# Performance work log

Measured on AMD Instinct MI355X. Metric: run time of the kernel, lower is better.

## Reference

```python
import jax, jax.numpy as jnp
import numpy as np

VOCAB, EMB, ATT = 100000, 128, 128
N_CODES, N_ANC = 100000, 8

def setup_inputs() -> dict:
    key = jax.random.key(0)
    k1, k2, k3, k4, k5 = jax.random.split(key, 5)
    return {
        "W_emb": jax.random.normal(k1, (VOCAB, EMB), dtype=jnp.float32),
        "W_attention": jax.random.normal(k2, (2 * EMB, ATT), dtype=jnp.float32) * 0.05,
        "b_attention": jnp.zeros((ATT,), dtype=jnp.float32),
        "v_attention": jax.random.normal(k3, (ATT,), dtype=jnp.float32) * 0.05,
        "leaves": jax.random.randint(k4, (N_CODES, N_ANC), 0, VOCAB, dtype=jnp.int64),
        "ancestors": jax.random.randint(k5, (N_CODES, N_ANC), 0, VOCAB, dtype=jnp.int64),
    }

def reference(W_emb, W_attention, b_attention, v_attention, leaves, ancestors):
    # gather: [N, A, E] each
    leave_emb = W_emb[leaves]
    anc_emb = W_emb[ancestors]
    attention_input = jnp.concatenate((leave_emb, anc_emb), axis=2)  # [N, A, 2E]
    mlp = jnp.tanh(jnp.einsum('nae,ed->nad', attention_input, W_attention) + b_attention)
    pre_attention = jnp.einsum('nad,d->na', mlp, v_attention)  # [N, A]
    attn = jax.nn.softmax(pre_attention, axis=1)
    # attention-weighted sum over ancestors: [N, E]
    return jnp.einsum('nae,na->ne', anc_emb, attn)
```

## Files before the change

### kernel.cpp

```cpp
#include <hip/hip_runtime.h>
#include <hip/hip_bf16.h>

#define VOCAB  100000
#define EMB    128
#define NCODES 100000
#define NANC   8
#define PAD    136

typedef __attribute__((ext_vector_type(8))) short  short8;
typedef __attribute__((ext_vector_type(4))) float  float4v;

__device__ __forceinline__ ushort f2bf(float x) {
    unsigned u = __float_as_uint(x);
    u += 0x7fffu + ((u >> 16) & 1u);
    return (ushort)(u >> 16);
}
__device__ __forceinline__ float bf2f(ushort h) {
    return __uint_as_float((unsigned)h << 16);
}
__device__ __forceinline__ float tanh_fast(float x) {
    float e = __expf(2.0f * x);
    return 1.0f - __fdividef(2.0f, e + 1.0f);
}

__global__ __launch_bounds__(256) void precompute(
    const float* __restrict__ W_emb,
    const float* __restrict__ W_att,
    const float* __restrict__ b_att,
    ushort* __restrict__ P1, ushort* __restrict__ P2, ushort* __restrict__ Ebf)
{
    __shared__ ushort sBT[256 * PAD];
    const int t = threadIdx.x;

    {
        const int tg = t >> 7;
        const int c  = t & 127;
        for (int rr = 0; rr < 128; rr += 2) {
            const int r = tg * 128 + rr;
            ushort2 pk;
            pk.x = f2bf(W_att[r * 128 + c]);
            pk.y = f2bf(W_att[(r + 1) * 128 + c]);
            *(ushort2*)&sBT[(tg * 128 + c) * PAD + rr] = pk;
        }
    }
    __syncthreads();

    const int wave = t >> 6, lane = t & 63;
    const int n15 = lane & 15, quad = lane >> 4;
    const long arow = (long)blockIdx.x * 64 + wave * 16 + n15;
    const long arc  = arow < VOCAB ? arow : 0;

    float4v acc[16];
    #pragma unroll
    for (int i = 0; i < 16; ++i) acc[i] = (float4v)0.0f;

    #pragma unroll
    for (int kt = 0; kt < 4; ++kt) {
        const float4* src = (const float4*)(W_emb + arc * 128 + kt * 32 + quad * 8);
        const float4 a0 = src[0], a1 = src[1];
        short8 af;
        af[0] = f2bf(a0.x); af[1] = f2bf(a0.y); af[2] = f2bf(a0.z); af[3] = f2bf(a0.w);
        af[4] = f2bf(a1.x); af[5] = f2bf(a1.y); af[6] = f2bf(a1.z); af[7] = f2bf(a1.w);
        if (arow < VOCAB)
            *(short8*)(void*)(Ebf + arow * 128 + kt * 32 + quad * 8) = af;
        #pragma unroll
        for (int nt = 0; nt < 16; ++nt) {
            short8 bfr = *(const short8*)&sBT[(nt * 16 + n15) * PAD + kt * 32 + quad * 8];
            acc[nt] = __builtin_amdgcn_mfma_f32_16x16x32_bf16(af, bfr, acc[nt], 0, 0, 0);
        }
    }

    float bv[8];
    #pragma unroll
    for (int nt = 0; nt < 8; ++nt) bv[nt] = b_att[nt * 16 + n15];

    const long srow0 = (long)blockIdx.x * 64 + wave * 16 + quad * 4;
    #pragma unroll
    for (int nt = 0; nt < 16; ++nt) {
        const int cc = nt * 16 + n15;
        #pragma unroll
        for (int i = 0; i < 4; ++i) {
            const long gr = srow0 + i;
            if (gr < VOCAB) {
                const float v = acc[nt][i] + (nt < 8 ? bv[nt] : 0.0f);
                const ushort h = f2bf(v);
                if (nt < 8) P1[gr * 128 + cc]       = h;
                else        P2[gr * 128 + cc - 128] = h;
            }
        }
    }
}

__global__ __launch_bounds__(256) void attention_main(
    const ushort* __restrict__ P1, const ushort* __restrict__ P2,
    const ushort* __restrict__ Ebf,
    const float* __restrict__ v_att,
    const int*   __restrict__ leaves, const int* __restrict__ anc,
    float*       __restrict__ out)
{
    const int lane = threadIdx.x & 63;
    const int wave = threadIdx.x >> 6;
    const int h    = lane >> 5, l32 = lane & 31;
    const long n   = ((long)blockIdx.x * 4 + wave) * 2 + h;

    const float4 vv = *(const float4*)(v_att + l32 * 4);

    int lidx = 0;
    if (l32 < 16)
        lidx = (l32 < 8) ? leaves[n * 8 + l32] : anc[n * 8 + (l32 & 7)];

    ushort4 emb[NANC];
    float q[NANC];
    #pragma unroll
    for (int a = 0; a < NANC; ++a) {
        const int lf = __shfl(lidx, h * 32 + a);
        const int an = __shfl(lidx, h * 32 + 8 + a);
        const ushort4 r1 = *(const ushort4*)(P1  + (size_t)lf * 128 + l32 * 4);
        const ushort4 r2 = *(const ushort4*)(P2  + (size_t)an * 128 + l32 * 4);
        emb[a]           = *(const ushort4*)(Ebf + (size_t)an * 128 + l32 * 4);
        const float z0 = bf2f(r1.x) + bf2f(r2.x);
        const float z1 = bf2f(r1.y) + bf2f(r2.y);
        const float z2 = bf2f(r1.z) + bf2f(r2.z);
        const float z3 = bf2f(r1.w) + bf2f(r2.w);
        float qp = tanh_fast(z0) * vv.x + tanh_fast(z1) * vv.y
                 + tanh_fast(z2) * vv.z + tanh_fast(z3) * vv.w;
        qp += __shfl_xor(qp, 1); qp += __shfl_xor(qp, 2);
        qp += __shfl_xor(qp, 4); qp += __shfl_xor(qp, 8);
        qp += __shfl_xor(qp, 16);
        q[a] = qp;
    }

    float m = q[0];
    #pragma unroll
    for (int a = 1; a < NANC; ++a) m = fmaxf(m, q[a]);
    float s = 0.f, w[NANC];
    #pragma unroll
    for (int a = 0; a < NANC; ++a) { w[a] = __expf(q[a] - m); s += w[a]; }
    const float inv = __fdividef(1.0f, s);

    float4 o = make_float4(0.f, 0.f, 0.f, 0.f);
    #pragma unroll
    for (int a = 0; a < NANC; ++a) {
        const float wa = w[a] * inv;
        o.x = fmaf(wa, bf2f(emb[a].x), o.x);
        o.y = fmaf(wa, bf2f(emb[a].y), o.y);
        o.z = fmaf(wa, bf2f(emb[a].z), o.z);
        o.w = fmaf(wa, bf2f(emb[a].w), o.w);
    }
    *(float4*)(out + (size_t)n * 128 + l32 * 4) = o;
}

extern "C" void kernel_launch(void* const* d_in, const int* in_sizes, int n_in,
                              void* d_out, int out_size, void* d_ws, size_t ws_size,
                              hipStream_t stream) {
    const float* W_emb  = (const float*)d_in[0];
    const float* W_att  = (const float*)d_in[1];
    const float* b_att  = (const float*)d_in[2];
    const float* v_att  = (const float*)d_in[3];
    const int*   leaves = (const int*)d_in[4];
    const int*   anc    = (const int*)d_in[5];
    float*       out    = (float*)d_out;

    ushort* P1  = (ushort*)d_ws;
    ushort* P2  = P1 + (size_t)VOCAB * 128;
    ushort* Ebf = P2 + (size_t)VOCAB * 128;

    precompute<<<(VOCAB + 63) / 64, 256, 0, stream>>>(W_emb, W_att, b_att,
                                                      P1, P2, Ebf);
    attention_main<<<NCODES / 8, 256, 0, stream>>>(P1, P2, Ebf, v_att,
                                                   leaves, anc, out);
}
```

Measured before the change: 231.6 us.

## Store projections in FP8, retile precompute, and regroup attention lanes per code

```diff
diff --git a/kernel.cpp b/kernel.cpp
--- a/kernel.cpp
+++ b/kernel.cpp
@@ -1,14 +1,15 @@
 #include <hip/hip_runtime.h>
 #include <hip/hip_bf16.h>
+#include <hip/hip_fp8.h>
 
 #define VOCAB  100000
 #define EMB    128
 #define NCODES 100000
 #define NANC   8
-#define PAD    136
 
 typedef __attribute__((ext_vector_type(8))) short  short8;
 typedef __attribute__((ext_vector_type(4))) float  float4v;
+typedef __attribute__((ext_vector_type(2))) float  floatx2;
 
 __device__ __forceinline__ ushort f2bf(float x) {
     unsigned u = __float_as_uint(x);
@@ -22,132 +23,195 @@
     float e = __expf(2.0f * x);
     return 1.0f - __fdividef(2.0f, e + 1.0f);
 }
+__device__ __forceinline__ unsigned char f2fp8(float x) {
+    __hip_fp8_e4m3 t(x);
+    return t.__x;
+}
+template <bool HI>
+__device__ __forceinline__ floatx2 fp8pair(unsigned v) {
+#if __has_builtin(__builtin_amdgcn_cvt_pk_f32_fp8)
+    return __builtin_amdgcn_cvt_pk_f32_fp8((int)v, HI);
+#else
+    __hip_fp8_e4m3 a, b;
+    const unsigned s = HI ? 16u : 0u;
+    a.__x = (v >> s) & 0xffu;
+    b.__x = (v >> (s + 8u)) & 0xffu;
+    floatx2 r; r[0] = (float)a; r[1] = (float)b; return r;
+#endif
+}
+
+__global__ void transpose_watt(const float* __restrict__ W_att,
+                               ushort* __restrict__ WT)
+{
+    const int id = blockIdx.x * 256 + threadIdx.x;
+    const int c = id >> 7, e = id & 127;
+    const int h = c >> 7, d = c & 127;
+    WT[c * 128 + e] = f2bf(W_att[(h * 128 + e) * 128 + d]);
+}
 
 __global__ __launch_bounds__(256) void precompute(
-    const float* __restrict__ W_emb,
-    const float* __restrict__ W_att,
-    const float* __restrict__ b_att,
-    ushort* __restrict__ P1, ushort* __restrict__ P2, ushort* __restrict__ Ebf)
+    const float*  __restrict__ W_emb,
+    const ushort* __restrict__ WT,
+    const float*  __restrict__ b_att,
+    unsigned char* __restrict__ P1,
+    unsigned char* __restrict__ P2,
+    ushort*        __restrict__ Ebf)
 {
-    __shared__ ushort sBT[256 * PAD];
-    const int t = threadIdx.x;
-
-    {
-        const int tg = t >> 7;
-        const int c  = t & 127;
-        for (int rr = 0; rr < 128; rr += 2) {
-            const int r = tg * 128 + rr;
-            ushort2 pk;
-            pk.x = f2bf(W_att[r * 128 + c]);
-            pk.y = f2bf(W_att[(r + 1) * 128 + c]);
-            *(ushort2*)&sBT[(tg * 128 + c) * PAD + rr] = pk;
-        }
-    }
-    __syncthreads();
-
-    const int wave = t >> 6, lane = t & 63;
+    const int t = threadIdx.x, wave = t >> 6, lane = t & 63;
     const int n15 = lane & 15, quad = lane >> 4;
-    const long arow = (long)blockIdx.x * 64 + wave * 16 + n15;
-    const long arc  = arow < VOCAB ? arow : 0;
-
-    float4v acc[16];
-    #pragma unroll
-    for (int i = 0; i < 16; ++i) acc[i] = (float4v)0.0f;
+    const int R = blockIdx.x * 16;
+
+    short8 bfrag[4][4];
+    #pragma unroll
+    for (int ntl = 0; ntl < 4; ++ntl) {
+        const int c = wave * 64 + ntl * 16 + n15;
+        #pragma unroll
+        for (int kt = 0; kt < 4; ++kt)
+            bfrag[kt][ntl] = *(const short8*)(WT + c * 128 + kt * 32 + quad * 8);
+    }
+
+    float4v acc[4];
+    #pragma unroll
+    for (int i = 0; i < 4; ++i) acc[i] = (float4v)0.0f;
 
     #pragma unroll
     for (int kt = 0; kt < 4; ++kt) {
-        const float4* src = (const float4*)(W_emb + arc * 128 + kt * 32 + quad * 8);
+        const float4* src = (const float4*)(W_emb + (size_t)(R + n15) * 128
+                                            + kt * 32 + quad * 8);
         const float4 a0 = src[0], a1 = src[1];
         short8 af;
         af[0] = f2bf(a0.x); af[1] = f2bf(a0.y); af[2] = f2bf(a0.z); af[3] = f2bf(a0.w);
         af[4] = f2bf(a1.x); af[5] = f2bf(a1.y); af[6] = f2bf(a1.z); af[7] = f2bf(a1.w);
-        if (arow < VOCAB)
-            *(short8*)(void*)(Ebf + arow * 128 + kt * 32 + quad * 8) = af;
-        #pragma unroll
-        for (int nt = 0; nt < 16; ++nt) {
-            short8 bfr = *(const short8*)&sBT[(nt * 16 + n15) * PAD + kt * 32 + quad * 8];
-            acc[nt] = __builtin_amdgcn_mfma_f32_16x16x32_bf16(af, bfr, acc[nt], 0, 0, 0);
+        if (wave == 0)
+            __builtin_nontemporal_store(af,
+                (short8*)(Ebf + (size_t)(R + n15) * 128 + kt * 32 + quad * 8));
+        #pragma unroll
+        for (int ntl = 0; ntl < 4; ++ntl)
+            acc[ntl] = __builtin_amdgcn_mfma_f32_16x16x32_bf16(
+                           af, bfrag[kt][ntl], acc[ntl], 0, 0, 0);
+    }
+
+    const int cw = wave * 64;
+    float bv[4] = {0.f, 0.f, 0.f, 0.f};
+    if (wave < 2) {
+        #pragma unroll
+        for (int ntl = 0; ntl < 4; ++ntl) bv[ntl] = b_att[cw + ntl * 16 + n15];
+    }
+    unsigned char* Pt = (wave < 2) ? P1 : P2;
+    const int cofs = (wave < 2) ? cw : cw - 128;
+    #pragma unroll
+    for (int ntl = 0; ntl < 4; ++ntl) {
+        const int c = cofs + ntl * 16 + n15;
+        #pragma unroll
+        for (int i = 0; i < 4; ++i) {
+            const int r = R + quad * 4 + i;
+            __builtin_nontemporal_store(f2fp8(acc[ntl][i] + bv[ntl]),
+                                        Pt + (size_t)r * 128 + c);
         }
     }
-
-    float bv[8];
-    #pragma unroll
-    for (int nt = 0; nt < 8; ++nt) bv[nt] = b_att[nt * 16 + n15];
-
-    const long srow0 = (long)blockIdx.x * 64 + wave * 16 + quad * 4;
-    #pragma unroll
-    for (int nt = 0; nt < 16; ++nt) {
-        const int cc = nt * 16 + n15;
-        #pragma unroll
-        for (int i = 0; i < 4; ++i) {
-            const long gr = srow0 + i;
-            if (gr < VOCAB) {
-                const float v = acc[nt][i] + (nt < 8 ? bv[nt] : 0.0f);
-                const ushort h = f2bf(v);
-                if (nt < 8) P1[gr * 128 + cc]       = h;
-                else        P2[gr * 128 + cc - 128] = h;
-            }
-        }
-    }
 }
 
 __global__ __launch_bounds__(256) void attention_main(
-    const ushort* __restrict__ P1, const ushort* __restrict__ P2,
+    const unsigned char* __restrict__ P1, const unsigned char* __restrict__ P2,
     const ushort* __restrict__ Ebf,
     const float* __restrict__ v_att,
     const int*   __restrict__ leaves, const int* __restrict__ anc,
     float*       __restrict__ out)
 {
-    const int lane = threadIdx.x & 63;
-    const int wave = threadIdx.x >> 6;
-    const int h    = lane >> 5, l32 = lane & 31;
-    const long n   = ((long)blockIdx.x * 4 + wave) * 2 + h;
-
-    const float4 vv = *(const float4*)(v_att + l32 * 4);
-
-    int lidx = 0;
-    if (l32 < 16)
-        lidx = (l32 < 8) ? leaves[n * 8 + l32] : anc[n * 8 + (l32 & 7)];
-
-    ushort4 emb[NANC];
+    const int t = threadIdx.x;
+    const int wave = t >> 6, lane = t & 63;
+    const int sub = lane >> 4, l16 = lane & 15;
+    const int n = blockIdx.x * 16 + wave * 4 + sub;
+
+    const float4 vva = *(const float4*)(v_att + l16 * 8);
+    const float4 vvb = *(const float4*)(v_att + l16 * 8 + 4);
+
+    const int jj = l16 & 7;
+    const int lidx = (l16 & 8) ? anc[n * 8 + jj] : leaves[n * 8 + jj];
+
+    short8 em[NANC];
     float q[NANC];
     #pragma unroll
     for (int a = 0; a < NANC; ++a) {
-        const int lf = __shfl(lidx, h * 32 + a);
-        const int an = __shfl(lidx, h * 32 + 8 + a);
-        const ushort4 r1 = *(const ushort4*)(P1  + (size_t)lf * 128 + l32 * 4);
-        const ushort4 r2 = *(const ushort4*)(P2  + (size_t)an * 128 + l32 * 4);
-        emb[a]           = *(const ushort4*)(Ebf + (size_t)an * 128 + l32 * 4);
-        const float z0 = bf2f(r1.x) + bf2f(r2.x);
-        const float z1 = bf2f(r1.y) + bf2f(r2.y);
-        const float z2 = bf2f(r1.z) + bf2f(r2.z);
-        const float z3 = bf2f(r1.w) + bf2f(r2.w);
-        float qp = tanh_fast(z0) * vv.x + tanh_fast(z1) * vv.y
-                 + tanh_fast(z2) * vv.z + tanh_fast(z3) * vv.w;
-        qp += __shfl_xor(qp, 1); qp += __shfl_xor(qp, 2);
-        qp += __shfl_xor(qp, 4); qp += __shfl_xor(qp, 8);
-        qp += __shfl_xor(qp, 16);
+        const int lf = __shfl(lidx, (sub << 4) + a);
+        const int an = __shfl(lidx, (sub << 4) + 8 + a);
+        const uint2 r1 = *(const uint2*)(P1 + (size_t)lf * 128 + l16 * 8);
+        const uint2 r2 = *(const uint2*)(P2 + (size_t)an * 128 + l16 * 8);
+        em[a] = *(const short8*)(Ebf + (size_t)an * 128 + l16 * 8);
+        floatx2 pa, pb;
+        float qp;
+        pa = fp8pair<false>(r1.x); pb = fp8pair<false>(r2.x);
+        qp  = tanh_fast(pa[0] + pb[0]) * vva.x;
+        qp  = fmaf(tanh_fast(pa[1] + pb[1]), vva.y, qp);
+        pa = fp8pair<true>(r1.x);  pb = fp8pair<true>(r2.x);
+        qp  = fmaf(tanh_fast(pa[0] + pb[0]), vva.z, qp);
+        qp  = fmaf(tanh_fast(pa[1] + pb[1]), vva.w, qp);
+        pa = fp8pair<false>(r1.y); pb = fp8pair<false>(r2.y);
+        qp  = fmaf(tanh_fast(pa[0] + pb[0]), vvb.x, qp);
+        qp  = fmaf(tanh_fast(pa[1] + pb[1]), vvb.y, qp);
+        pa = fp8pair<true>(r1.y);  pb = fp8pair<true>(r2.y);
+        qp  = fmaf(tanh_fast(pa[0] + pb[0]), vvb.z, qp);
+        qp  = fmaf(tanh_fast(pa[1] + pb[1]), vvb.w, qp);
         q[a] = qp;
     }
 
-    float m = q[0];
-    #pragma unroll
-    for (int a = 1; a < NANC; ++a) m = fmaxf(m, q[a]);
-    float s = 0.f, w[NANC];
-    #pragma unroll
-    for (int a = 0; a < NANC; ++a) { w[a] = __expf(q[a] - m); s += w[a]; }
-    const float inv = __fdividef(1.0f, s);
-
-    float4 o = make_float4(0.f, 0.f, 0.f, 0.f);
+    float r4[4];
+    #pragma unroll
+    for (int i = 0; i < 4; ++i) {
+        const float keep = (l16 & 8) ? q[i + 4] : q[i];
+        const float send = (l16 & 8) ? q[i]     : q[i + 4];
+        r4[i] = keep + __shfl_xor(send, 8);
+    }
+    float s2[2];
+    #pragma unroll
+    for (int i = 0; i < 2; ++i) {
+        const float keep = (l16 & 4) ? r4[i + 2] : r4[i];
+        const float send = (l16 & 4) ? r4[i]     : r4[i + 2];
+        s2[i] = keep + __shfl_xor(send, 4);
+    }
+    {
+        const float keep = (l16 & 2) ? s2[1] : s2[0];
+        const float send = (l16 & 2) ? s2[0] : s2[1];
+        s2[0] = keep + __shfl_xor(send, 2);
+    }
+    float tq = s2[0] + __shfl_xor(s2[0], 1);
+
+    float m = tq;
+    m = fmaxf(m, __shfl_xor(m, 8));
+    m = fmaxf(m, __shfl_xor(m, 4));
+    m = fmaxf(m, __shfl_xor(m, 2));
+    const float e = __expf(tq - m);
+    float s = e;
+    s += __shfl_xor(s, 8); s += __shfl_xor(s, 4); s += __shfl_xor(s, 2);
+    const float wl = e * __fdividef(1.0f, s);
+
+    float wa[NANC];
+    {
+        const float p  = __shfl_xor(wl, 2);
+        const float w0 = (l16 & 2) ? p  : wl;
+        const float w1 = (l16 & 2) ? wl : p;
+        const float p0 = __shfl_xor(w0, 4), p1 = __shfl_xor(w1, 4);
+        const float v00 = (l16 & 4) ? p0 : w0, v01 = (l16 & 4) ? p1 : w1;
+        const float v10 = (l16 & 4) ? w0 : p0, v11 = (l16 & 4) ? w1 : p1;
+        float g;
+        g = __shfl_xor(v00, 8); wa[0] = (l16 & 8) ? g : v00; wa[4] = (l16 & 8) ? v00 : g;
+        g = __shfl_xor(v01, 8); wa[1] = (l16 & 8) ? g : v01; wa[5] = (l16 & 8) ? v01 : g;
+        g = __shfl_xor(v10, 8); wa[2] = (l16 & 8) ? g : v10; wa[6] = (l16 & 8) ? v10 : g;
+        g = __shfl_xor(v11, 8); wa[3] = (l16 & 8) ? g : v11; wa[7] = (l16 & 8) ? v11 : g;
+    }
+
+    float o[8] = {0.f, 0.f, 0.f, 0.f, 0.f, 0.f, 0.f, 0.f};
     #pragma unroll
     for (int a = 0; a < NANC; ++a) {
-        const float wa = w[a] * inv;
-        o.x = fmaf(wa, bf2f(emb[a].x), o.x);
-        o.y = fmaf(wa, bf2f(emb[a].y), o.y);
-        o.z = fmaf(wa, bf2f(emb[a].z), o.z);
-        o.w = fmaf(wa, bf2f(emb[a].w), o.w);
-    }
-    *(float4*)(out + (size_t)n * 128 + l32 * 4) = o;
+        #pragma unroll
+        for (int c = 0; c < 8; ++c)
+            o[c] = fmaf(wa[a], bf2f((ushort)em[a][c]), o[c]);
+    }
+    float4v o1, o2;
+    o1[0] = o[0]; o1[1] = o[1]; o1[2] = o[2]; o1[3] = o[3];
+    o2[0] = o[4]; o2[1] = o[5]; o2[2] = o[6]; o2[3] = o[7];
+    __builtin_nontemporal_store(o1, (float4v*)(out + (size_t)n * 128 + l16 * 8));
+    __builtin_nontemporal_store(o2, (float4v*)(out + (size_t)n * 128 + l16 * 8 + 4));
 }
 
 extern "C" void kernel_launch(void* const* d_in, const int* in_sizes, int n_in,
@@ -161,12 +225,13 @@
     const int*   anc    = (const int*)d_in[5];
     float*       out    = (float*)d_out;
 
-    ushort* P1  = (ushort*)d_ws;
-    ushort* P2  = P1 + (size_t)VOCAB * 128;
-    ushort* Ebf = P2 + (size_t)VOCAB * 128;
-
-    precompute<<<(VOCAB + 63) / 64, 256, 0, stream>>>(W_emb, W_att, b_att,
-                                                      P1, P2, Ebf);
-    attention_main<<<NCODES / 8, 256, 0, stream>>>(P1, P2, Ebf, v_att,
-                                                   leaves, anc, out);
-}
+    unsigned char* P1 = (unsigned char*)d_ws;
+    unsigned char* P2 = P1 + (size_t)VOCAB * 128;
+    ushort* Ebf = (ushort*)(P2 + (size_t)VOCAB * 128);
+    ushort* WT  = Ebf + (size_t)VOCAB * 128;
+
+    transpose_watt<<<128, 256, 0, stream>>>(W_att, WT);
+    precompute<<<VOCAB / 16, 256, 0, stream>>>(W_emb, WT, b_att, P1, P2, Ebf);
+    attention_main<<<NCODES / 16, 256, 0, stream>>>(P1, P2, Ebf, v_att,
+                                                    leaves, anc, out);
+}
```

After: 243.1 us. +5.0%, slower.
